# Kernel optimization log

Hardware: AMD Instinct MI355X
Metric: run time of the kernel (lower is better)

## Reference

```python
import jax, jax.numpy as jnp
import numpy as np

B, T, C = 2, 2048, 1024
H = 16
D = C // H  # 64

def setup_inputs() -> dict:
    key = jax.random.key(0)
    k1, k2, k3 = jax.random.split(key, 3)
    s = 0.02
    return {
        "x": jax.random.normal(k1, (B, T, C), dtype=jnp.float32),
        "Wqkv": jax.random.normal(k2, (C, 3 * C), dtype=jnp.float32) * s,
        "bqkv": jnp.zeros((3 * C,), dtype=jnp.float32),
        "Wproj": jax.random.normal(k3, (C, C), dtype=jnp.float32) * s,
        "bproj": jnp.zeros((C,), dtype=jnp.float32),
    }

def reference(x, Wqkv, bqkv, Wproj, bproj):
    b, t, c = x.shape
    qkv = x @ Wqkv + bqkv                       # [B,T,3C]
    qkv = qkv.reshape(b, t, 3, H, D)
    q = qkv[:, :, 0].transpose(0, 2, 1, 3)      # [B,H,T,D]
    k = qkv[:, :, 1].transpose(0, 2, 1, 3)
    v = qkv[:, :, 2].transpose(0, 2, 1, 3)
    scale = 1.0 / np.sqrt(D).astype(np.float32)
    att = jnp.einsum('bhqd,bhkd->bhqk', q, k) * scale  # [B,H,T,T]
    causal = jnp.tril(jnp.ones((t, t), dtype=bool))
    att = jnp.where(causal[None, None], att, jnp.float32(-jnp.inf))
    att = jax.nn.softmax(att, axis=-1)
    y = jnp.einsum('bhqk,bhkd->bhqd', att, v)   # [B,H,T,D]
    y = y.transpose(0, 2, 1, 3).reshape(b, t, c)
    return y @ Wproj + bproj
```

## Files before the change

### kernel.cpp

```cpp
#include <hip/hip_runtime.h>

typedef __bf16 bf16x8 __attribute__((ext_vector_type(8)));
typedef float  f32x4  __attribute__((ext_vector_type(4)));
typedef float  f32x16 __attribute__((ext_vector_type(16)));
typedef unsigned int uint32x4 __attribute__((ext_vector_type(4)));

__device__ __forceinline__ short f2bf(float f) {
  union { float f; unsigned u; } v; v.f = f;
  unsigned r = v.u + 0x7fffu + ((v.u >> 16) & 1u);
  return (short)(r >> 16);
}

__device__ __forceinline__ void gl_lds16(const short* g, short* l) {
  __builtin_amdgcn_global_load_lds((const __attribute__((address_space(1))) void*)g,
                                   (__attribute__((address_space(3))) void*)l, 16, 0, 0);
}

__global__ __launch_bounds__(256) void cast_x_kernel(const float* __restrict__ in,
                                                     short* __restrict__ out, int n4) {
  int i = blockIdx.x * 256 + threadIdx.x;
  if (i >= n4) return;
  float4 f = reinterpret_cast<const float4*>(in)[i];
  short4 o;
  o.x = f2bf(f.x); o.y = f2bf(f.y); o.z = f2bf(f.z); o.w = f2bf(f.w);
  reinterpret_cast<short4*>(out)[i] = o;
}

__global__ __launch_bounds__(256) void transpose_cast(const float* __restrict__ in,
                                                      short* __restrict__ out, int R, int Cc) {
  __shared__ short tile[64][65];
  int bx = blockIdx.x * 64;
  int by = blockIdx.y * 64;
  int tx = threadIdx.x & 63, ty = threadIdx.x >> 6;
  #pragma unroll
  for (int i = ty; i < 64; i += 4)
    tile[i][tx] = f2bf(in[(size_t)(by + i) * Cc + bx + tx]);
  __syncthreads();
  #pragma unroll
  for (int i = ty; i < 64; i += 4)
    out[(size_t)(bx + i) * R + by + tx] = tile[tx][i];
}


__global__ __launch_bounds__(256, 3) void gemm_qkv(const short* __restrict__ A,
                                                   const short* __restrict__ Bt,
                                                   const float* __restrict__ bias,
                                                   short* __restrict__ qo,
                                                   short* __restrict__ ko,
                                                   short* __restrict__ vt) {
  const int K = 1024;
  __shared__ short smem[24576];
  int tid = threadIdx.x;
  int ntile = blockIdx.x * 64, mtile = blockIdx.y * 128;
  int w = tid >> 6, l = tid & 63;
  int lr = l & 15, lg = l >> 4;

  f32x4 zero4 = {0.f, 0.f, 0.f, 0.f};
  f32x4 acc[2][4];
  #pragma unroll
  for (int i = 0; i < 2; ++i)
    #pragma unroll
    for (int j = 0; j < 4; ++j) acc[i][j] = zero4;

#define STAGE_QKV(BUF, K0) do {                                                      \
    short* Ab_ = smem + (BUF) * 12288;                                               \
    short* Bb_ = Ab_ + 8192;                                                         \
    _Pragma("unroll")                                                                \
    for (int c = 0; c < 4; ++c) {                                                    \
      int idx = tid + c * 256;                                                       \
      int row = idx >> 3, kc = idx & 7;                                              \
      gl_lds16(&A[(size_t)(mtile + row) * K + (K0) + kc * 8], &Ab_[idx * 8]);        \
    }                                                                                \
    _Pragma("unroll")                                                                \
    for (int c = 0; c < 2; ++c) {                                                    \
      int idx = tid + c * 256;                                                       \
      int row = idx >> 3, kc = idx & 7;                                              \
      gl_lds16(&Bt[(size_t)(ntile + row) * K + (K0) + kc * 8], &Bb_[idx * 8]);       \
    }                                                                                \
  } while (0)

  STAGE_QKV(0, 0);
  __syncthreads();
  int cur = 0;
  for (int it = 0; it < 16; ++it) {
    if (it < 15) STAGE_QKV(cur ^ 1, (it + 1) * 64);
    const short* Ab = smem + cur * 12288;
    const short* Bb = Ab + 8192;
    __builtin_amdgcn_s_setprio(1);
    #pragma unroll
    for (int kk = 0; kk < 2; ++kk) {
      bf16x8 af[2], bfr[4];
      #pragma unroll
      for (int i = 0; i < 2; ++i)
        af[i] = *reinterpret_cast<const bf16x8*>(&Ab[(w * 32 + i * 16 + lr) * 64 + kk * 32 + lg * 8]);
      #pragma unroll
      for (int j = 0; j < 4; ++j)
        bfr[j] = *reinterpret_cast<const bf16x8*>(&Bb[(j * 16 + lr) * 64 + kk * 32 + lg * 8]);
      #pragma unroll
      for (int i = 0; i < 2; ++i)
        #pragma unroll
        for (int j = 0; j < 4; ++j)
          acc[i][j] = __builtin_amdgcn_mfma_f32_16x16x32_bf16(af[i], bfr[j], acc[i][j], 0, 0, 0);
    }
    __builtin_amdgcn_s_setprio(0);
    __syncthreads();
    cur ^= 1;
  }
#undef STAGE_QKV

  const int sec = ntile >> 10;
  if (sec == 2) {
    #pragma unroll
    for (int j = 0; j < 4; ++j) {
      int d = j * 16 + lr;
      float bv = bias[ntile + d];
      #pragma unroll
      for (int i = 0; i < 2; ++i) {
        int lt0 = w * 32 + i * 16 + lg * 4;
        int pos = (((lt0 >> 3) & 1) << 10) + (d & 31) * 32 +
                  ((((lt0 >> 4) & 1) + ((d >> 5) << 1)) << 3) + (lt0 & 7);
        short4 pk;
        pk.x = f2bf(acc[i][j][0] + bv);
        pk.y = f2bf(acc[i][j][1] + bv);
        pk.z = f2bf(acc[i][j][2] + bv);
        pk.w = f2bf(acc[i][j][3] + bv);
        *reinterpret_cast<short4*>(&smem[(lt0 >> 5) * 2048 + pos]) = pk;
      }
    }
  } else {
    const float sc = (sec == 0) ? 0.18033688f : 1.0f;
    #pragma unroll
    for (int j = 0; j < 4; ++j) {
      int d = j * 16 + lr;
      float bv = bias[ntile + d];
      int dpart = (((d >> 3) & 1) << 10) + ((d >> 4) << 3) + (d & 7);
      #pragma unroll
      for (int i = 0; i < 2; ++i) {
        #pragma unroll
        for (int r = 0; r < 4; ++r) {
          int lt = w * 32 + i * 16 + lg * 4 + r;
          smem[(lt >> 5) * 2048 + (lt & 31) * 32 + dpart] = f2bf((acc[i][j][r] + bv) * sc);
        }
      }
    }
  }
  __syncthreads();
  short* dst = (sec == 0) ? qo : ((sec == 1) ? ko : vt);
  int bb  = mtile >> 11;
  int h0  = (ntile & 1023) >> 6;
  int gt0 = (mtile & 2047) >> 5;
  #pragma unroll
  for (int c2 = 0; c2 < 4; ++c2) {
    size_t base = (size_t)(bb * 16 + h0) * 131072 + (size_t)(gt0 + c2) * 2048;
    *reinterpret_cast<uint4*>(&dst[base + tid * 8]) =
        *reinterpret_cast<const uint4*>(&smem[c2 * 2048 + tid * 8]);
  }
}

template<int DIAG>
__device__ __forceinline__ void attn_step(const short* __restrict__ kp,
                                          const short* __restrict__ vp,
                                          const bf16x8* qf,
                                          f32x16& y0, f32x16& y1,
                                          float& m, float& li,
                                          int lq, int hl) {
  f32x16 s;
  #pragma unroll
  for (int r = 0; r < 16; ++r) s[r] = 0.f;
  __builtin_amdgcn_s_setprio(1);
  #pragma unroll
  for (int ks = 0; ks < 4; ++ks) {
    bf16x8 kf = *reinterpret_cast<const bf16x8*>(kp + ks * 8);
    s = __builtin_amdgcn_mfma_f32_32x32x16_bf16(kf, qf[ks], s, 0, 0, 0);
  }
  __builtin_amdgcn_s_setprio(0);
  if (DIAG) {
    #pragma unroll
    for (int r = 0; r < 16; ++r) {
      int kvl = (r & 3) + 8 * (r >> 2) + 4 * hl;
      if (kvl > lq) s[r] = -1e30f;
    }
  }
  float a0 = fmaxf(fmaxf(s[0], s[1]), fmaxf(s[2], s[3]));
  float a1 = fmaxf(fmaxf(s[4], s[5]), fmaxf(s[6], s[7]));
  float a2 = fmaxf(fmaxf(s[8], s[9]), fmaxf(s[10], s[11]));
  float a3 = fmaxf(fmaxf(s[12], s[13]), fmaxf(s[14], s[15]));
  float pm = fmaxf(fmaxf(a0, a1), fmaxf(a2, a3));
  pm = fmaxf(pm, __shfl_xor(pm, 32));
  if (!__all(pm - m <= 8.0f)) {
    float mn = fmaxf(m, pm);
    float sc = __builtin_amdgcn_exp2f(m - mn);
    m = mn;
    li *= sc;
    #pragma unroll
    for (int r = 0; r < 16; ++r) { y0[r] *= sc; y1[r] *= sc; }
  }
  unsigned u[8];
  float rs = 0.f;
  #pragma unroll
  for (int rq = 0; rq < 4; ++rq) {
    float p0 = __builtin_amdgcn_exp2f(s[4 * rq + 0] - m);
    float p1 = __builtin_amdgcn_exp2f(s[4 * rq + 1] - m);
    float p2 = __builtin_amdgcn_exp2f(s[4 * rq + 2] - m);
    float p3 = __builtin_amdgcn_exp2f(s[4 * rq + 3] - m);
    rs += (p0 + p1) + (p2 + p3);
    asm("v_cvt_pk_bf16_f32 %0, %1, %2" : "=v"(u[rq * 2 + 0]) : "v"(p0), "v"(p1));
    asm("v_cvt_pk_bf16_f32 %0, %1, %2" : "=v"(u[rq * 2 + 1]) : "v"(p2), "v"(p3));
  }
  rs += __shfl_xor(rs, 32);
  li += rs;
  asm volatile("v_permlane32_swap_b32 %0, %1" : "+v"(u[0]), "+v"(u[2]));
  asm volatile("v_permlane32_swap_b32 %0, %1" : "+v"(u[1]), "+v"(u[3]));
  asm volatile("v_permlane32_swap_b32 %0, %1" : "+v"(u[4]), "+v"(u[6]));
  asm volatile("v_permlane32_swap_b32 %0, %1" : "+v"(u[5]), "+v"(u[7]));
  uint32x4 w0 = {u[0], u[1], u[2], u[3]};
  uint32x4 w1 = {u[4], u[5], u[6], u[7]};
  bf16x8 pa0 = __builtin_bit_cast(bf16x8, w0);
  bf16x8 pa1 = __builtin_bit_cast(bf16x8, w1);
  __builtin_amdgcn_s_setprio(1);
  {
    bf16x8 vf00 = *reinterpret_cast<const bf16x8*>(vp);
    bf16x8 vf01 = *reinterpret_cast<const bf16x8*>(vp + 8);
    bf16x8 vf10 = *reinterpret_cast<const bf16x8*>(vp + 16);
    bf16x8 vf11 = *reinterpret_cast<const bf16x8*>(vp + 24);
    y0 = __builtin_amdgcn_mfma_f32_32x32x16_bf16(vf00, pa0, y0, 0, 0, 0);
    y0 = __builtin_amdgcn_mfma_f32_32x32x16_bf16(vf01, pa1, y0, 0, 0, 0);
    y1 = __builtin_amdgcn_mfma_f32_32x32x16_bf16(vf10, pa0, y1, 0, 0, 0);
    y1 = __builtin_amdgcn_mfma_f32_32x32x16_bf16(vf11, pa1, y1, 0, 0, 0);
  }
  __builtin_amdgcn_s_setprio(0);
}

__global__ __launch_bounds__(256, 4) void attn_kernel(const short* __restrict__ q,
                                                      const short* __restrict__ k,
                                                      const short* __restrict__ vt,
                                                      short* __restrict__ y) {
  __shared__ float partL[3][4][64][4];
  __shared__ float stm[4][32], stl[4][32];
  const int bid = blockIdx.x;
  const int t = 63 - (bid >> 5);
  const int b5 = bid & 31;
  const int bh = (b5 & 7) * 4 + (b5 >> 3);
  const int tid = threadIdx.x;
  const int w = tid >> 6;
  const int l = tid & 63;
  const int lq = l & 31, hl = l >> 5;
  const short* qb = q + (size_t)bh * 131072;
  const short* kb = k + (size_t)bh * 131072;
  const short* vb = vt + (size_t)bh * 131072;

  bf16x8 qf[4];
  {
    const short* qp = qb + (size_t)t * 2048 + l * 32;
    #pragma unroll
    for (int ks = 0; ks < 4; ++ks)
      qf[ks] = *reinterpret_cast<const bf16x8*>(qp + ks * 8);
  }

  f32x16 y0, y1;
  #pragma unroll
  for (int r = 0; r < 16; ++r) { y0[r] = 0.f; y1[r] = 0.f; }
  float m = -1e30f, li = 0.f;

  const short* kp = kb + (size_t)w * 2048 + l * 32;
  const short* vp = vb + (size_t)w * 2048 + l * 32;
  for (int it = w; it < t; it += 4) {
    attn_step<0>(kp, vp, qf, y0, y1, m, li, lq, hl);
    kp += 4 * 2048;
    vp += 4 * 2048;
  }
  if ((t & 3) == w) {
    const short* kpd = kb + (size_t)t * 2048 + l * 32;
    const short* vpd = vb + (size_t)t * 2048 + l * 32;
    attn_step<1>(kpd, vpd, qf, y0, y1, m, li, lq, hl);
  }

  if (hl == 0) { stm[w][lq] = m; stl[w][lq] = li; }
  __syncthreads();
  float m0 = stm[0][lq], m1 = stm[1][lq], m2 = stm[2][lq], m3 = stm[3][lq];
  float M = fmaxf(fmaxf(m0, m1), fmaxf(m2, m3));
  float L = stl[0][lq] * __builtin_amdgcn_exp2f(m0 - M) +
            stl[1][lq] * __builtin_amdgcn_exp2f(m1 - M) +
            stl[2][lq] * __builtin_amdgcn_exp2f(m2 - M) +
            stl[3][lq] * __builtin_amdgcn_exp2f(m3 - M);
  float sc = __builtin_amdgcn_exp2f(m - M);
  #pragma unroll
  for (int r = 0; r < 16; ++r) { y0[r] *= sc; y1[r] *= sc; }

  if (w > 0) {
    #pragma unroll
    for (int c = 0; c < 4; ++c) {
      f32x4 v0 = {y0[4 * c + 0], y0[4 * c + 1], y0[4 * c + 2], y0[4 * c + 3]};
      *reinterpret_cast<f32x4*>(&partL[w - 1][c][l][0]) = v0;
    }
  }
  __syncthreads();
  if (w == 0) {
    #pragma unroll
    for (int o = 0; o < 3; ++o)
      #pragma unroll
      for (int c = 0; c < 4; ++c) {
        f32x4 v0 = *reinterpret_cast<const f32x4*>(&partL[o][c][l][0]);
        #pragma unroll
        for (int r = 0; r < 4; ++r) y0[4 * c + r] += v0[r];
      }
  }
  __syncthreads();
  if (w > 0) {
    #pragma unroll
    for (int c = 0; c < 4; ++c) {
      f32x4 v1 = {y1[4 * c + 0], y1[4 * c + 1], y1[4 * c + 2], y1[4 * c + 3]};
      *reinterpret_cast<f32x4*>(&partL[w - 1][c][l][0]) = v1;
    }
  }
  __syncthreads();
  if (w == 0) {
    #pragma unroll
    for (int o = 0; o < 3; ++o)
      #pragma unroll
      for (int c = 0; c < 4; ++c) {
        f32x4 v1 = *reinterpret_cast<const f32x4*>(&partL[o][c][l][0]);
        #pragma unroll
        for (int r = 0; r < 4; ++r) y1[4 * c + r] += v1[r];
      }
    float inv = 1.0f / L;
    int b_ = bh >> 4, h_ = bh & 15;
    short* yrow = &y[(size_t)(b_ * 2048 + 32 * t + lq) * 1024 + h_ * 64];
    #pragma unroll
    for (int dt = 0; dt < 2; ++dt) {
      const f32x16& yy = dt ? y1 : y0;
      #pragma unroll
      for (int rq = 0; rq < 4; ++rq) {
        int d0 = dt * 32 + 8 * rq + 4 * hl;
        uint2 pk;
        pk.x = (unsigned)(unsigned short)f2bf(yy[4 * rq + 0] * inv) |
               ((unsigned)(unsigned short)f2bf(yy[4 * rq + 1] * inv) << 16);
        pk.y = (unsigned)(unsigned short)f2bf(yy[4 * rq + 2] * inv) |
               ((unsigned)(unsigned short)f2bf(yy[4 * rq + 3] * inv) << 16);
        *reinterpret_cast<uint2*>(yrow + d0) = pk;
      }
    }
  }
}

__global__ __launch_bounds__(256, 3) void gemm_proj(const short* __restrict__ A,
                                                    const short* __restrict__ Bt,
                                                    const float* __restrict__ bias,
                                                    float* __restrict__ out) {
  const int K = 1024;
  __shared__ short smem[24576];
  int tid = threadIdx.x;
  int ntile = blockIdx.x * 64, mtile = blockIdx.y * 128;
  int w = tid >> 6, l = tid & 63;
  int lr = l & 15, lg = l >> 4;

  f32x4 zero4 = {0.f, 0.f, 0.f, 0.f};
  f32x4 acc[2][4];
  #pragma unroll
  for (int i = 0; i < 2; ++i)
    #pragma unroll
    for (int j = 0; j < 4; ++j) acc[i][j] = zero4;

#define STAGE_PRJ(BUF, K0) do {                                                      \
    short* Ab_ = smem + (BUF) * 12288;                                               \
    short* Bb_ = Ab_ + 8192;                                                         \
    _Pragma("unroll")                                                                \
    for (int c = 0; c < 4; ++c) {                                                    \
      int idx = tid + c * 256;                                                       \
      int row = idx >> 3, kc = idx & 7;                                              \
      gl_lds16(&A[(size_t)(mtile + row) * K + (K0) + kc * 8], &Ab_[idx * 8]);        \
    }                                                                                \
    _Pragma("unroll")                                                                \
    for (int c = 0; c < 2; ++c) {                                                    \
      int idx = tid + c * 256;                                                       \
      int row = idx >> 3, kc = idx & 7;                                              \
      gl_lds16(&Bt[(size_t)(ntile + row) * K + (K0) + kc * 8], &Bb_[idx * 8]);       \
    }                                                                                \
  } while (0)

  STAGE_PRJ(0, 0);
  __syncthreads();
  int cur = 0;
  for (int it = 0; it < 16; ++it) {
    if (it < 15) STAGE_PRJ(cur ^ 1, (it + 1) * 64);
    const short* Ab = smem + cur * 12288;
    const short* Bb = Ab + 8192;
    __builtin_amdgcn_s_setprio(1);
    #pragma unroll
    for (int kk = 0; kk < 2; ++kk) {
      bf16x8 af[2], bfr[4];
      #pragma unroll
      for (int i = 0; i < 2; ++i)
        af[i] = *reinterpret_cast<const bf16x8*>(&Ab[(w * 32 + i * 16 + lr) * 64 + kk * 32 + lg * 8]);
      #pragma unroll
      for (int j = 0; j < 4; ++j)
        bfr[j] = *reinterpret_cast<const bf16x8*>(&Bb[(j * 16 + lr) * 64 + kk * 32 + lg * 8]);
      #pragma unroll
      for (int i = 0; i < 2; ++i)
        #pragma unroll
        for (int j = 0; j < 4; ++j)
          acc[i][j] = __builtin_amdgcn_mfma_f32_16x16x32_bf16(af[i], bfr[j], acc[i][j], 0, 0, 0);
    }
    __builtin_amdgcn_s_setprio(0);
    __syncthreads();
    cur ^= 1;
  }
#undef STAGE_PRJ

  #pragma unroll
  for (int j = 0; j < 4; ++j) {
    int n = ntile + j * 16 + lr;
    float bv = bias[n];
    #pragma unroll
    for (int i = 0; i < 2; ++i) {
      #pragma unroll
      for (int r = 0; r < 4; ++r) {
        int m = mtile + w * 32 + i * 16 + lg * 4 + r;
        out[(size_t)m * 1024 + n] = acc[i][j][r] + bv;
      }
    }
  }
}

extern "C" void kernel_launch(void* const* d_in, const int* in_sizes, int n_in,
                              void* d_out, int out_size, void* d_ws, size_t ws_size,
                              hipStream_t stream) {
  const float* x     = (const float*)d_in[0];
  const float* Wqkv  = (const float*)d_in[1];
  const float* bqkv  = (const float*)d_in[2];
  const float* Wproj = (const float*)d_in[3];
  const float* bproj = (const float*)d_in[4];
  float* out = (float*)d_out;

  const size_t M4 = 4096ull * 1024ull;
  short* ws = (short*)d_ws;
  short* x_bf    = ws;
  short* wqkv_t  = ws + M4;
  short* wproj_t = ws + M4 + 3ull * 1024 * 1024;
  short* qb      = wproj_t + 1024ull * 1024;
  short* kb      = qb + M4;
  short* vtb     = kb + M4;
  short* yb      = x_bf;

  cast_x_kernel<<<4096, 256, 0, stream>>>(x, x_bf, (int)(M4 / 4));
  transpose_cast<<<dim3(48, 16), 256, 0, stream>>>(Wqkv, wqkv_t, 1024, 3072);
  transpose_cast<<<dim3(16, 16), 256, 0, stream>>>(Wproj, wproj_t, 1024, 1024);
  gemm_qkv<<<dim3(48, 32), 256, 0, stream>>>(x_bf, wqkv_t, bqkv, qb, kb, vtb);
  attn_kernel<<<2048, 256, 0, stream>>>(qb, kb, vtb, yb);
  gemm_proj<<<dim3(16, 32), 256, 0, stream>>>(yb, wproj_t, bproj, out);
}
```

Measured before the change: 122.1 us.

## Enlarge QKV GEMM tile to 128x128 and remap block indices for XCD locality

The QKV projection GEMM now computes 128x128 output tiles per block, with a 2x2 warp grid each holding 4x4 MFMA accumulators, instead of 128x64. This halves the A-operand reloads and raises arithmetic intensity, at the cost of more LDS and registers, so the launch bound drops to 2 blocks per CU. Both GEMMs now use a 1D grid whose block index is remapped so that consecutive blocks on the same XCD (blockIdx & 7) share M rows and nearby N tiles, improving L2 reuse. The epilogue is extended to write two heads per block.

```diff
diff --git a/kernel.cpp b/kernel.cpp
--- a/kernel.cpp
+++ b/kernel.cpp
@@ -42,39 +42,37 @@
 }
 
 
-__global__ __launch_bounds__(256, 3) void gemm_qkv(const short* __restrict__ A,
+__global__ __launch_bounds__(256, 2) void gemm_qkv(const short* __restrict__ A,
                                                    const short* __restrict__ Bt,
                                                    const float* __restrict__ bias,
                                                    short* __restrict__ qo,
                                                    short* __restrict__ ko,
                                                    short* __restrict__ vt) {
   const int K = 1024;
-  __shared__ short smem[24576];
+  __shared__ short smem[32768];
   int tid = threadIdx.x;
-  int ntile = blockIdx.x * 64, mtile = blockIdx.y * 128;
+  int x = blockIdx.x & 7, r = blockIdx.x >> 3;
+  int mt = r / 3, ntl = r - mt * 3;
+  int ntile = (x * 3 + ntl) * 128, mtile = mt * 128;
   int w = tid >> 6, l = tid & 63;
+  int wr = w >> 1, wc = w & 1;
   int lr = l & 15, lg = l >> 4;
 
   f32x4 zero4 = {0.f, 0.f, 0.f, 0.f};
-  f32x4 acc[2][4];
-  #pragma unroll
-  for (int i = 0; i < 2; ++i)
+  f32x4 acc[4][4];
+  #pragma unroll
+  for (int i = 0; i < 4; ++i)
     #pragma unroll
     for (int j = 0; j < 4; ++j) acc[i][j] = zero4;
 
 #define STAGE_QKV(BUF, K0) do {                                                      \
-    short* Ab_ = smem + (BUF) * 12288;                                               \
+    short* Ab_ = smem + (BUF) * 16384;                                               \
     short* Bb_ = Ab_ + 8192;                                                         \
     _Pragma("unroll")                                                                \
     for (int c = 0; c < 4; ++c) {                                                    \
       int idx = tid + c * 256;                                                       \
       int row = idx >> 3, kc = idx & 7;                                              \
       gl_lds16(&A[(size_t)(mtile + row) * K + (K0) + kc * 8], &Ab_[idx * 8]);        \
-    }                                                                                \
-    _Pragma("unroll")                                                                \
-    for (int c = 0; c < 2; ++c) {                                                    \
-      int idx = tid + c * 256;                                                       \
-      int row = idx >> 3, kc = idx & 7;                                              \
       gl_lds16(&Bt[(size_t)(ntile + row) * K + (K0) + kc * 8], &Bb_[idx * 8]);       \
     }                                                                                \
   } while (0)
@@ -84,20 +82,20 @@
   int cur = 0;
   for (int it = 0; it < 16; ++it) {
     if (it < 15) STAGE_QKV(cur ^ 1, (it + 1) * 64);
-    const short* Ab = smem + cur * 12288;
+    const short* Ab = smem + cur * 16384;
     const short* Bb = Ab + 8192;
     __builtin_amdgcn_s_setprio(1);
     #pragma unroll
     for (int kk = 0; kk < 2; ++kk) {
-      bf16x8 af[2], bfr[4];
-      #pragma unroll
-      for (int i = 0; i < 2; ++i)
-        af[i] = *reinterpret_cast<const bf16x8*>(&Ab[(w * 32 + i * 16 + lr) * 64 + kk * 32 + lg * 8]);
+      bf16x8 af[4], bfr[4];
+      #pragma unroll
+      for (int i = 0; i < 4; ++i)
+        af[i] = *reinterpret_cast<const bf16x8*>(&Ab[(wr * 64 + i * 16 + lr) * 64 + kk * 32 + lg * 8]);
       #pragma unroll
       for (int j = 0; j < 4; ++j)
-        bfr[j] = *reinterpret_cast<const bf16x8*>(&Bb[(j * 16 + lr) * 64 + kk * 32 + lg * 8]);
-      #pragma unroll
-      for (int i = 0; i < 2; ++i)
+        bfr[j] = *reinterpret_cast<const bf16x8*>(&Bb[(wc * 64 + j * 16 + lr) * 64 + kk * 32 + lg * 8]);
+      #pragma unroll
+      for (int i = 0; i < 4; ++i)
         #pragma unroll
         for (int j = 0; j < 4; ++j)
           acc[i][j] = __builtin_amdgcn_mfma_f32_16x16x32_bf16(af[i], bfr[j], acc[i][j], 0, 0, 0);
@@ -112,11 +110,13 @@
   if (sec == 2) {
     #pragma unroll
     for (int j = 0; j < 4; ++j) {
-      int d = j * 16 + lr;
-      float bv = bias[ntile + d];
-      #pragma unroll
-      for (int i = 0; i < 2; ++i) {
-        int lt0 = w * 32 + i * 16 + lg * 4;
+      int nl = wc * 64 + j * 16 + lr;
+      int d  = nl & 63;
+      float bv = bias[ntile + nl];
+      #pragma unroll
+      for (int i = 0; i < 4; ++i) {
+        int lt0 = wr * 64 + i * 16 + lg * 4;
+        int c2 = (nl >> 6) * 4 + (lt0 >> 5);
         int pos = (((lt0 >> 3) & 1) << 10) + (d & 31) * 32 +
                   ((((lt0 >> 4) & 1) + ((d >> 5) << 1)) << 3) + (lt0 & 7);
         short4 pk;
@@ -124,22 +124,24 @@
         pk.y = f2bf(acc[i][j][1] + bv);
         pk.z = f2bf(acc[i][j][2] + bv);
         pk.w = f2bf(acc[i][j][3] + bv);
-        *reinterpret_cast<short4*>(&smem[(lt0 >> 5) * 2048 + pos]) = pk;
+        *reinterpret_cast<short4*>(&smem[c2 * 2048 + pos]) = pk;
       }
     }
   } else {
     const float sc = (sec == 0) ? 0.18033688f : 1.0f;
     #pragma unroll
     for (int j = 0; j < 4; ++j) {
-      int d = j * 16 + lr;
-      float bv = bias[ntile + d];
+      int nl = wc * 64 + j * 16 + lr;
+      int d  = nl & 63;
+      float bv = bias[ntile + nl];
       int dpart = (((d >> 3) & 1) << 10) + ((d >> 4) << 3) + (d & 7);
       #pragma unroll
-      for (int i = 0; i < 2; ++i) {
+      for (int i = 0; i < 4; ++i) {
         #pragma unroll
-        for (int r = 0; r < 4; ++r) {
-          int lt = w * 32 + i * 16 + lg * 4 + r;
-          smem[(lt >> 5) * 2048 + (lt & 31) * 32 + dpart] = f2bf((acc[i][j][r] + bv) * sc);
+        for (int r2 = 0; r2 < 4; ++r2) {
+          int lt = wr * 64 + i * 16 + lg * 4 + r2;
+          int c2 = (nl >> 6) * 4 + (lt >> 5);
+          smem[c2 * 2048 + (lt & 31) * 32 + dpart] = f2bf((acc[i][j][r2] + bv) * sc);
         }
       }
     }
@@ -150,8 +152,9 @@
   int h0  = (ntile & 1023) >> 6;
   int gt0 = (mtile & 2047) >> 5;
   #pragma unroll
-  for (int c2 = 0; c2 < 4; ++c2) {
-    size_t base = (size_t)(bb * 16 + h0) * 131072 + (size_t)(gt0 + c2) * 2048;
+  for (int c2 = 0; c2 < 8; ++c2) {
+    size_t base = (size_t)(bb * 16 + h0 + (c2 >> 2)) * 131072 +
+                  (size_t)(gt0 + (c2 & 3)) * 2048;
     *reinterpret_cast<uint4*>(&dst[base + tid * 8]) =
         *reinterpret_cast<const uint4*>(&smem[c2 * 2048 + tid * 8]);
   }
@@ -350,7 +353,8 @@
   const int K = 1024;
   __shared__ short smem[24576];
   int tid = threadIdx.x;
-  int ntile = blockIdx.x * 64, mtile = blockIdx.y * 128;
+  int x = blockIdx.x & 7, r = blockIdx.x >> 3;
+  int ntile = (x * 2 + (r & 1)) * 64, mtile = (r >> 1) * 128;
   int w = tid >> 6, l = tid & 63;
   int lr = l & 15, lg = l >> 4;
 
@@ -414,9 +418,9 @@
     #pragma unroll
     for (int i = 0; i < 2; ++i) {
       #pragma unroll
-      for (int r = 0; r < 4; ++r) {
-        int m = mtile + w * 32 + i * 16 + lg * 4 + r;
-        out[(size_t)m * 1024 + n] = acc[i][j][r] + bv;
+      for (int r2 = 0; r2 < 4; ++r2) {
+        int m = mtile + w * 32 + i * 16 + lg * 4 + r2;
+        out[(size_t)m * 1024 + n] = acc[i][j][r2] + bv;
       }
     }
   }
@@ -445,7 +449,7 @@
   cast_x_kernel<<<4096, 256, 0, stream>>>(x, x_bf, (int)(M4 / 4));
   transpose_cast<<<dim3(48, 16), 256, 0, stream>>>(Wqkv, wqkv_t, 1024, 3072);
   transpose_cast<<<dim3(16, 16), 256, 0, stream>>>(Wproj, wproj_t, 1024, 1024);
-  gemm_qkv<<<dim3(48, 32), 256, 0, stream>>>(x_bf, wqkv_t, bqkv, qb, kb, vtb);
+  gemm_qkv<<<768, 256, 0, stream>>>(x_bf, wqkv_t, bqkv, qb, kb, vtb);
   attn_kernel<<<2048, 256, 0, stream>>>(qb, kb, vtb, yb);
-  gemm_proj<<<dim3(16, 32), 256, 0, stream>>>(yb, wproj_t, bproj, out);
-}
+  gemm_proj<<<512, 256, 0, stream>>>(yb, wproj_t, bproj, out);
+}
```

Result: no change. 120.2 us (-1.6%).
